# Kernel optimization log

Measured on AMD Instinct MI355X. Metric: run time of the kernel, lower is better.

Reference implementation:

```python
import jax, jax.numpy as jnp
import numpy as np
from jax import lax


def hard_sigmoid(x):
    # Keras hard_sigmoid: clip(0.2*x + 0.5, 0, 1)
    return jnp.clip(0.2 * x + 0.5, 0.0, 1.0)


def setup_inputs() -> dict:
    key = jax.random.key(0)
    ks = jax.random.split(key, 5)
    B, T, D, U, N = 256, 128, 256, 512, 2
    x = jax.random.normal(ks[0], (B, T, D), dtype=jnp.float32)
    h0 = jnp.zeros((B, U), dtype=jnp.float32)
    kernel = jax.random.normal(ks[1], (D, 5 * U), dtype=jnp.float32) * (1.0 / np.sqrt(D))
    recurrent_kernel = jax.random.normal(ks[2], (U, 4 * U), dtype=jnp.float32) * (1.0 / np.sqrt(U))
    t_kernels = jax.random.normal(ks[3], (N, U, 3 * U), dtype=jnp.float32) * (1.0 / np.sqrt(U))
    bias = jnp.zeros((2, 5 * U), dtype=jnp.float32)
    t_bias = jnp.zeros((N, 3 * U), dtype=jnp.float32)
    return {"x": x, "h0": h0, "kernel": kernel, "recurrent_kernel": recurrent_kernel,
            "t_kernels": t_kernels, "bias": bias, "t_bias": t_bias}


def reference(x, h0, kernel, recurrent_kernel, t_kernels, bias, t_bias):
    # x: [B,T,D]; h0: [B,U]; kernel: [D,5U]; recurrent_kernel: [U,4U]
    # t_kernels: [N,U,3U]; bias: [2,5U]; t_bias: [N,3U]
    U = h0.shape[-1]
    N = t_kernels.shape[0]  # static python int
    input_bias = bias[0]          # [5U]
    recurrent_bias = bias[1][:4 * U]  # [4U]

    # Precompute all input projections once: [B,T,5U]
    xg_all = jnp.einsum('btd,dg->btg', x, kernel) + input_bias

    def step(h, xg):
        # xg: [B,5U]
        xz, xr, xh, xl, xl2 = (xg[:, i * U:(i + 1) * U] for i in range(5))
        hg = h @ recurrent_kernel + recurrent_bias  # [B,4U]
        hz, hr, hhr, hl = (hg[:, i * U:(i + 1) * U] for i in range(4))
        z = hard_sigmoid(xz + hz)
        r = hard_sigmoid(xr + hr)
        hh = jnp.tanh(xh + r * hhr)  # reset_after=True convention
        h1 = z * h + (1.0 - z) * hh
        # tree-cell chain: recurrent-only GRU sub-updates
        for i in range(N):
            tg = h1 @ t_kernels[i] + t_bias[i]  # [B,3U]
            tz, tr, th = tg[:, :U], tg[:, U:2 * U], tg[:, 2 * U:3 * U]
            zt = hard_sigmoid(tz)
            rt = hard_sigmoid(tr)
            ht = jnp.tanh(rt * th)
            h1 = zt * h1 + (1.0 - zt) * ht
        # leak gates from the extra myl/myl2 kernels
        l = hard_sigmoid(xl + hl)
        h_out = l * h1 + (1.0 - l) * jnp.tanh(xl2)
        return h_out, h_out

    _, ys = lax.scan(step, h0, xg_all.transpose(1, 0, 2))  # ys: [T,B,U]
    return ys.transpose(1, 0, 2)  # [B,T,U]
```

## Files before the change

### kernel.cpp

```cpp
#include <hip/hip_runtime.h>
#include <math.h>

#define BB 256
#define TT 128
#define DD 256
#define UU 512
#define G5 (5 * UU)
#define G4 (4 * UU)
#define NBLK 256
#define GBLK 32

__device__ __forceinline__ float hsig(float x) {
    return fminf(fmaxf(0.2f * x + 0.5f, 0.0f), 1.0f);
}

__device__ __forceinline__ void st_sys(float* p, float v) {
    __hip_atomic_store(p, v, __ATOMIC_RELAXED, __HIP_MEMORY_SCOPE_SYSTEM);
}
__device__ __forceinline__ float ld_sys(const float* p) {
    return __hip_atomic_load(p, __ATOMIC_RELAXED, __HIP_MEMORY_SCOPE_SYSTEM);
}

__global__ __launch_bounds__(256) void pack_weights(
    const float* __restrict__ rk, const float* __restrict__ tk,
    float* __restrict__ rkp, float* __restrict__ tkp0, float* __restrict__ tkp1)
{
    int idx = blockIdx.x * 256 + threadIdx.x;
    int k = idx >> 11;
    int c = idx & 2047;
    int u = c >> 2;
    int g = c & 3;
    rkp[idx] = rk[k * G4 + g * UU + u];
    float t0 = 0.f, t1 = 0.f;
    if (g < 3) {
        t0 = tk[(size_t)k * (3 * UU) + g * UU + u];
        t1 = tk[(size_t)(UU + k) * (3 * UU) + g * UU + u];
    }
    tkp0[idx] = t0;
    tkp1[idx] = t1;
}

__global__ __launch_bounds__(256) void init_hT(
    const float* __restrict__ h0, float* __restrict__ hT)
{
    int idx = blockIdx.x * 256 + threadIdx.x;
    int u = idx >> 8;
    int b = idx & 255;
    hT[idx] = h0[(size_t)b * UU + u];
}

__device__ __forceinline__ void gbar(unsigned* cnt, unsigned& phase) {
    __syncthreads();
    if (threadIdx.x == 0) {
        phase += GBLK;
        __hip_atomic_fetch_add(cnt, 1u, __ATOMIC_RELAXED, __HIP_MEMORY_SCOPE_AGENT);
        while ((int)(__hip_atomic_load(cnt, __ATOMIC_RELAXED, __HIP_MEMORY_SCOPE_AGENT) - phase) < 0)
            __builtin_amdgcn_s_sleep(2);
        __builtin_amdgcn_fence(__ATOMIC_ACQUIRE, "workgroup");
    }
    __syncthreads();
    __builtin_amdgcn_sched_barrier(0);
}

__device__ __forceinline__ void rt_gemm(
    const float* __restrict__ AT,
    const float* __restrict__ Wp,
    int bm, int bn, int tid,
    float (* __restrict__ As)[36], float (* __restrict__ Ws)[80],
    float* __restrict__ RedF,
    float* __restrict__ s, int& row_out)
{
    const int lane = tid & 63;
    const int kg = tid >> 6;
    const int r8 = lane & 7;
    const int c8 = lane >> 3;
    const int akr = tid >> 3;
    const int amc = (tid & 7) * 4;
    const int wwr = tid >> 4;
    const int wwc = (tid & 15) * 4;

    const float* ap = AT + (size_t)akr * BB + bm + amc;
    const float* wp = Wp + (size_t)wwr * G4 + bn + wwc;

    float a0[4], a1[4];
#pragma unroll
    for (int j = 0; j < 4; ++j) {
        a0[j] = ld_sys(ap + j);
        a1[j] = ld_sys(ap + 32 * BB + j);
    }
    float4 w0 = *(const float4*)wp;
    float4 w1 = *(const float4*)(wp + 16 * G4);
    float4 w2 = *(const float4*)(wp + 32 * G4);
    float4 w3 = *(const float4*)(wp + 48 * G4);

    float acc[4][8];
#pragma unroll
    for (int r = 0; r < 4; ++r)
#pragma unroll
        for (int j = 0; j < 8; ++j) acc[r][j] = 0.f;

#pragma unroll 1
    for (int tile = 0; tile < 8; ++tile) {
        __syncthreads();
        As[akr][amc + 0] = a0[0]; As[akr][amc + 1] = a0[1];
        As[akr][amc + 2] = a0[2]; As[akr][amc + 3] = a0[3];
        As[akr + 32][amc + 0] = a1[0]; As[akr + 32][amc + 1] = a1[1];
        As[akr + 32][amc + 2] = a1[2]; As[akr + 32][amc + 3] = a1[3];
        *(float4*)&Ws[wwr][wwc] = w0;
        *(float4*)&Ws[wwr + 16][wwc] = w1;
        *(float4*)&Ws[wwr + 32][wwc] = w2;
        *(float4*)&Ws[wwr + 48][wwc] = w3;
        if (tile < 7) {
            ap += 64 * BB;
            wp += 64 * G4;
#pragma unroll
            for (int j = 0; j < 4; ++j) {
                a0[j] = ld_sys(ap + j);
                a1[j] = ld_sys(ap + 32 * BB + j);
            }
            w0 = *(const float4*)wp;
            w1 = *(const float4*)(wp + 16 * G4);
            w2 = *(const float4*)(wp + 32 * G4);
            w3 = *(const float4*)(wp + 48 * G4);
        }
        __syncthreads();
        const int kb = kg * 16;
#pragma unroll
        for (int q = 0; q < 16; ++q) {
            float4 av4 = *(const float4*)&As[kb + q][r8 * 4];
            float4 wv0 = *(const float4*)&Ws[kb + q][c8 * 8];
            float4 wv1 = *(const float4*)&Ws[kb + q][c8 * 8 + 4];
            float av[4] = {av4.x, av4.y, av4.z, av4.w};
            float wv[8] = {wv0.x, wv0.y, wv0.z, wv0.w, wv1.x, wv1.y, wv1.z, wv1.w};
#pragma unroll
            for (int r = 0; r < 4; ++r)
#pragma unroll
                for (int j = 0; j < 8; ++j)
                    acc[r][j] += av[r] * wv[j];
        }
    }

#pragma unroll
    for (int r = 0; r < 4; ++r)
#pragma unroll
        for (int j = 0; j < 8; ++j)
            RedF[(kg * 32 + r * 8 + j) * 64 + lane] = acc[r][j];
    __syncthreads();
#pragma unroll
    for (int j = 0; j < 8; ++j)
        s[j] = RedF[(kg * 8 + j) * 64 + lane]
             + RedF[(32 + kg * 8 + j) * 64 + lane]
             + RedF[(64 + kg * 8 + j) * 64 + lane]
             + RedF[(96 + kg * 8 + j) * 64 + lane];
    row_out = bm + r8 * 4 + kg;
}

__device__ __forceinline__ void xg_phase(
    const float* __restrict__ x, const float* __restrict__ Wxg,
    const float* __restrict__ bias0, float* __restrict__ xgdst, int t,
    int bm, int bnx, int tid,
    float (* __restrict__ As)[36], float (* __restrict__ Ws)[80],
    float* __restrict__ RedF)
{
    const int lane = tid & 63;
    const int kg = tid >> 6;
    const int r8 = lane & 7;
    const int c8 = lane >> 3;
    const int xbr = tid >> 3;
    const int xdc = (tid & 7) * 8;

    float acc[4][10];
#pragma unroll
    for (int r = 0; r < 4; ++r)
#pragma unroll
        for (int c = 0; c < 10; ++c) acc[r][c] = 0.f;

    const float* xrow = x + ((size_t)(bm + xbr) * TT + t) * DD;

#pragma unroll 1
    for (int tile = 0; tile < 4; ++tile) {
        const int k0 = tile * 64;
        float4 xa0 = *(const float4*)(xrow + k0 + xdc);
        float4 xa1 = *(const float4*)(xrow + k0 + xdc + 4);
        float4 wv[5];
#pragma unroll
        for (int l = 0; l < 5; ++l) {
            int idx = tid + l * 256;
            int wrow = idx / 20;
            int wcol = (idx % 20) * 4;
            wv[l] = *(const float4*)(Wxg + (size_t)(k0 + wrow) * G5 + bnx + wcol);
        }
        __syncthreads();
        As[xdc + 0][xbr] = xa0.x; As[xdc + 1][xbr] = xa0.y;
        As[xdc + 2][xbr] = xa0.z; As[xdc + 3][xbr] = xa0.w;
        As[xdc + 4][xbr] = xa1.x; As[xdc + 5][xbr] = xa1.y;
        As[xdc + 6][xbr] = xa1.z; As[xdc + 7][xbr] = xa1.w;
#pragma unroll
        for (int l = 0; l < 5; ++l) {
            int idx = tid + l * 256;
            int wrow = idx / 20;
            int wcol = (idx % 20) * 4;
            *(float4*)&Ws[wrow][wcol] = wv[l];
        }
        __syncthreads();
        const int kb = kg * 16;
#pragma unroll
        for (int q = 0; q < 16; ++q) {
            float4 av4 = *(const float4*)&As[kb + q][r8 * 4];
            float4 wv0 = *(const float4*)&Ws[kb + q][c8 * 8];
            float4 wv1 = *(const float4*)&Ws[kb + q][c8 * 8 + 4];
            float2 wv2 = *(const float2*)&Ws[kb + q][64 + c8 * 2];
            float av[4] = {av4.x, av4.y, av4.z, av4.w};
            float wvv[10] = {wv0.x, wv0.y, wv0.z, wv0.w,
                             wv1.x, wv1.y, wv1.z, wv1.w, wv2.x, wv2.y};
#pragma unroll
            for (int r = 0; r < 4; ++r)
#pragma unroll
                for (int c = 0; c < 10; ++c)
                    acc[r][c] += av[r] * wvv[c];
        }
    }

#pragma unroll
    for (int r = 0; r < 4; ++r)
#pragma unroll
        for (int c = 0; c < 10; ++c)
            RedF[(kg * 40 + r * 10 + c) * 64 + lane] = acc[r][c];
    __syncthreads();
    const int row = bm + r8 * 4 + kg;
#pragma unroll
    for (int c = 0; c < 10; ++c) {
        float sv = RedF[(kg * 10 + c) * 64 + lane]
                 + RedF[(40 + kg * 10 + c) * 64 + lane]
                 + RedF[(80 + kg * 10 + c) * 64 + lane]
                 + RedF[(120 + kg * 10 + c) * 64 + lane];
        int n = bnx + (c < 8 ? c8 * 8 + c : 64 + c8 * 2 + (c - 8));
        st_sys(&xgdst[(size_t)row * G5 + n], sv + bias0[n]);
    }
}

__global__ __launch_bounds__(256, 1) void scan_all(
    const float* __restrict__ x,
    const float* __restrict__ Wxg,
    const float* __restrict__ rkp,
    const float* __restrict__ tkp0,
    const float* __restrict__ tkp1,
    const float* __restrict__ bias,
    const float* __restrict__ tb,
    float* hT, float* h1aT, float* h1bT, float* prl,
    float* xg0, float* xg1, float* out, unsigned* bar)
{
    __shared__ float As[64][36];
    __shared__ float Ws[64][80];
    __shared__ float RedF[10240];

    const int tid = threadIdx.x;
    const int bid = blockIdx.x;
    const int bm = (bid >> 5) * 32;
    const int bn = (bid & 31) * 64;
    const int bnx = (bid & 31) * 80;
    const int lane = tid & 63;
    const int c8 = lane >> 3;
    const int ub = (bn >> 2) + c8 * 2;

    unsigned* cnt = bar + (bid >> 5) * 32;
    unsigned phase = 0;

    const float* bias0 = bias;
    const float* bias1 = bias + G5;
    const float* tb0 = tb;
    const float* tb1 = tb + 3 * UU;

    xg_phase(x, Wxg, bias0, xg0, 0, bm, bnx, tid, As, Ws, RedF);
    gbar(cnt, phase);

    float* xgc = xg0;
    float* xgn = xg1;

    for (int t = 0; t < TT; ++t) {
        {
            float s[8]; int row;
            rt_gemm(hT, rkp, bm, bn, tid, As, Ws, RedF, s, row);
            const float* xr_ = xgc + (size_t)row * G5;
#pragma unroll
            for (int uu = 0; uu < 2; ++uu) {
                int u = ub + uu;
                float z  = hsig(ld_sys(xr_ + u) + s[uu * 4 + 0] + bias1[u]);
                float r  = hsig(ld_sys(xr_ + UU + u) + s[uu * 4 + 1] + bias1[UU + u]);
                float hh = tanhf(ld_sys(xr_ + 2 * UU + u) + r * (s[uu * 4 + 2] + bias1[2 * UU + u]));
                float hold = ld_sys(&hT[(size_t)u * BB + row]);
                st_sys(&h1aT[(size_t)u * BB + row], z * hold + (1.f - z) * hh);
                st_sys(&prl[(size_t)row * UU + u],
                       ld_sys(xr_ + 3 * UU + u) + s[uu * 4 + 3] + bias1[3 * UU + u]);
            }
        }
        gbar(cnt, phase);

        {
            float s[8]; int row;
            rt_gemm(h1aT, tkp0, bm, bn, tid, As, Ws, RedF, s, row);
#pragma unroll
            for (int uu = 0; uu < 2; ++uu) {
                int u = ub + uu;
                float zt = hsig(s[uu * 4 + 0] + tb0[u]);
                float rt = hsig(s[uu * 4 + 1] + tb0[UU + u]);
                float ht = tanhf(rt * (s[uu * 4 + 2] + tb0[2 * UU + u]));
                float h1v = ld_sys(&h1aT[(size_t)u * BB + row]);
                st_sys(&h1bT[(size_t)u * BB + row], zt * h1v + (1.f - zt) * ht);
            }
        }
        if (t + 1 < TT)
            xg_phase(x, Wxg, bias0, xgn, t + 1, bm, bnx, tid, As, Ws, RedF);
        gbar(cnt, phase);

        {
            float s[8]; int row;
            rt_gemm(h1bT, tkp1, bm, bn, tid, As, Ws, RedF, s, row);
#pragma unroll
            for (int uu = 0; uu < 2; ++uu) {
                int u = ub + uu;
                float zt = hsig(s[uu * 4 + 0] + tb1[u]);
                float rt = hsig(s[uu * 4 + 1] + tb1[UU + u]);
                float ht = tanhf(rt * (s[uu * 4 + 2] + tb1[2 * UU + u]));
                float h1v = ld_sys(&h1bT[(size_t)u * BB + row]);
                float h2 = zt * h1v + (1.f - zt) * ht;
                float l = hsig(ld_sys(&prl[(size_t)row * UU + u]));
                float xl2 = ld_sys(&xgc[(size_t)row * G5 + 4 * UU + u]);
                float ho = l * h2 + (1.f - l) * tanhf(xl2);
                st_sys(&hT[(size_t)u * BB + row], ho);
                out[((size_t)row * TT + t) * UU + u] = ho;
            }
        }
        gbar(cnt, phase);

        float* tmp = xgc; xgc = xgn; xgn = tmp;
    }
}

extern "C" void kernel_launch(void* const* d_in, const int* in_sizes, int n_in,
                              void* d_out, int out_size, void* d_ws, size_t ws_size,
                              hipStream_t stream) {
    const float* x      = (const float*)d_in[0];
    const float* h0     = (const float*)d_in[1];
    const float* kernel = (const float*)d_in[2];
    const float* rk     = (const float*)d_in[3];
    const float* tk     = (const float*)d_in[4];
    const float* bias   = (const float*)d_in[5];
    const float* tb     = (const float*)d_in[6];
    float* out = (float*)d_out;

    unsigned* bar = (unsigned*)d_ws;
    float* base = (float*)d_ws + 256;
    float* rkp  = base;
    float* tkp0 = rkp  + (size_t)UU * G4;
    float* tkp1 = tkp0 + (size_t)UU * G4;
    float* hT   = tkp1 + (size_t)UU * G4;
    float* h1aT = hT   + (size_t)BB * UU;
    float* h1bT = h1aT + (size_t)BB * UU;
    float* prl  = h1bT + (size_t)BB * UU;
    float* xg0  = prl  + (size_t)BB * UU;
    float* xg1  = xg0  + (size_t)BB * G5;

    hipMemsetAsync(d_ws, 0, 1024, stream);
    pack_weights<<<dim3((UU * G4) / 256), dim3(256), 0, stream>>>(rk, tk, rkp, tkp0, tkp1);
    init_hT<<<dim3((BB * UU) / 256), dim3(256), 0, stream>>>(h0, hT);

    scan_all<<<dim3(NBLK), dim3(256), 0, stream>>>(
        x, kernel, rkp, tkp0, tkp1, bias, tb,
        hT, h1aT, h1bT, prl, xg0, xg1, out, bar);
}
```

Before: 9.495 ms.

## Halve batch rows per block and double the persistent grid to 512 blocks

Shrinks the per-block batch tile from 32 to 16 rows, so the persistent scan grid doubles to 512 blocks at two blocks per CU. Shared-memory tiles, register accumulators and the reduction are remapped so each thread produces one unit per row. This spreads each step's small GEMMs over more CUs and shortens per-block work between grid barriers. In exchange the recurrent weights are streamed twice as often across blocks, there are more barrier groups, and co-residency of all blocks is now required. A release fence is also added before the barrier increment.

New measurement: 14.47 ms. 52.4% more time.

```diff
diff --git a/kernel.cpp b/kernel.cpp
--- a/kernel.cpp
+++ b/kernel.cpp
@@ -7,8 +7,9 @@
 #define UU 512
 #define G5 (5 * UU)
 #define G4 (4 * UU)
-#define NBLK 256
+#define NBLK 512
 #define GBLK 32
+#define BMR 16
 
 __device__ __forceinline__ float hsig(float x) {
     return fminf(fmaxf(0.2f * x + 0.5f, 0.0f), 1.0f);
@@ -53,6 +54,7 @@
     __syncthreads();
     if (threadIdx.x == 0) {
         phase += GBLK;
+        __builtin_amdgcn_fence(__ATOMIC_RELEASE, "agent");
         __hip_atomic_fetch_add(cnt, 1u, __ATOMIC_RELAXED, __HIP_MEMORY_SCOPE_AGENT);
         while ((int)(__hip_atomic_load(cnt, __ATOMIC_RELAXED, __HIP_MEMORY_SCOPE_AGENT) - phase) < 0)
             __builtin_amdgcn_s_sleep(2);
@@ -66,46 +68,41 @@
     const float* __restrict__ AT,
     const float* __restrict__ Wp,
     int bm, int bn, int tid,
-    float (* __restrict__ As)[36], float (* __restrict__ Ws)[80],
+    float (* __restrict__ As)[20], float (* __restrict__ Ws)[80],
     float* __restrict__ RedF,
-    float* __restrict__ s, int& row_out)
+    float* __restrict__ s, int& row_out, int& u_out)
 {
     const int lane = tid & 63;
     const int kg = tid >> 6;
     const int r8 = lane & 7;
     const int c8 = lane >> 3;
-    const int akr = tid >> 3;
-    const int amc = (tid & 7) * 4;
+    const int akr = tid >> 2;
+    const int amc = (tid & 3) * 4;
     const int wwr = tid >> 4;
     const int wwc = (tid & 15) * 4;
 
     const float* ap = AT + (size_t)akr * BB + bm + amc;
     const float* wp = Wp + (size_t)wwr * G4 + bn + wwc;
 
-    float a0[4], a1[4];
-#pragma unroll
-    for (int j = 0; j < 4; ++j) {
-        a0[j] = ld_sys(ap + j);
-        a1[j] = ld_sys(ap + 32 * BB + j);
-    }
+    float a[4];
+#pragma unroll
+    for (int j = 0; j < 4; ++j) a[j] = ld_sys(ap + j);
     float4 w0 = *(const float4*)wp;
     float4 w1 = *(const float4*)(wp + 16 * G4);
     float4 w2 = *(const float4*)(wp + 32 * G4);
     float4 w3 = *(const float4*)(wp + 48 * G4);
 
-    float acc[4][8];
-#pragma unroll
-    for (int r = 0; r < 4; ++r)
+    float acc[2][8];
+#pragma unroll
+    for (int r = 0; r < 2; ++r)
 #pragma unroll
         for (int j = 0; j < 8; ++j) acc[r][j] = 0.f;
 
 #pragma unroll 1
     for (int tile = 0; tile < 8; ++tile) {
         __syncthreads();
-        As[akr][amc + 0] = a0[0]; As[akr][amc + 1] = a0[1];
-        As[akr][amc + 2] = a0[2]; As[akr][amc + 3] = a0[3];
-        As[akr + 32][amc + 0] = a1[0]; As[akr + 32][amc + 1] = a1[1];
-        As[akr + 32][amc + 2] = a1[2]; As[akr + 32][amc + 3] = a1[3];
+        float4 av4 = {a[0], a[1], a[2], a[3]};
+        *(float4*)&As[akr][amc] = av4;
         *(float4*)&Ws[wwr][wwc] = w0;
         *(float4*)&Ws[wwr + 16][wwc] = w1;
         *(float4*)&Ws[wwr + 32][wwc] = w2;
@@ -114,10 +111,7 @@
             ap += 64 * BB;
             wp += 64 * G4;
 #pragma unroll
-            for (int j = 0; j < 4; ++j) {
-                a0[j] = ld_sys(ap + j);
-                a1[j] = ld_sys(ap + 32 * BB + j);
-            }
+            for (int j = 0; j < 4; ++j) a[j] = ld_sys(ap + j);
             w0 = *(const float4*)wp;
             w1 = *(const float4*)(wp + 16 * G4);
             w2 = *(const float4*)(wp + 32 * G4);
@@ -127,51 +121,53 @@
         const int kb = kg * 16;
 #pragma unroll
         for (int q = 0; q < 16; ++q) {
-            float4 av4 = *(const float4*)&As[kb + q][r8 * 4];
+            float2 av = *(const float2*)&As[kb + q][r8 * 2];
             float4 wv0 = *(const float4*)&Ws[kb + q][c8 * 8];
             float4 wv1 = *(const float4*)&Ws[kb + q][c8 * 8 + 4];
-            float av[4] = {av4.x, av4.y, av4.z, av4.w};
             float wv[8] = {wv0.x, wv0.y, wv0.z, wv0.w, wv1.x, wv1.y, wv1.z, wv1.w};
 #pragma unroll
-            for (int r = 0; r < 4; ++r)
-#pragma unroll
-                for (int j = 0; j < 8; ++j)
-                    acc[r][j] += av[r] * wv[j];
-        }
-    }
-
-#pragma unroll
-    for (int r = 0; r < 4; ++r)
+            for (int j = 0; j < 8; ++j) {
+                acc[0][j] += av.x * wv[j];
+                acc[1][j] += av.y * wv[j];
+            }
+        }
+    }
+
+#pragma unroll
+    for (int r = 0; r < 2; ++r)
 #pragma unroll
         for (int j = 0; j < 8; ++j)
-            RedF[(kg * 32 + r * 8 + j) * 64 + lane] = acc[r][j];
+            RedF[(kg * 16 + r * 8 + j) * 64 + lane] = acc[r][j];
     __syncthreads();
-#pragma unroll
-    for (int j = 0; j < 8; ++j)
-        s[j] = RedF[(kg * 8 + j) * 64 + lane]
-             + RedF[(32 + kg * 8 + j) * 64 + lane]
-             + RedF[(64 + kg * 8 + j) * 64 + lane]
-             + RedF[(96 + kg * 8 + j) * 64 + lane];
-    row_out = bm + r8 * 4 + kg;
+    const int rr = kg & 1;
+    const int jb = (kg >> 1) * 4;
+#pragma unroll
+    for (int jj = 0; jj < 4; ++jj)
+        s[jj] = RedF[(rr * 8 + jb + jj) * 64 + lane]
+              + RedF[(16 + rr * 8 + jb + jj) * 64 + lane]
+              + RedF[(32 + rr * 8 + jb + jj) * 64 + lane]
+              + RedF[(48 + rr * 8 + jb + jj) * 64 + lane];
+    row_out = bm + r8 * 2 + rr;
+    u_out = (bn >> 2) + c8 * 2 + (kg >> 1);
 }
 
 __device__ __forceinline__ void xg_phase(
     const float* __restrict__ x, const float* __restrict__ Wxg,
     const float* __restrict__ bias0, float* __restrict__ xgdst, int t,
     int bm, int bnx, int tid,
-    float (* __restrict__ As)[36], float (* __restrict__ Ws)[80],
+    float (* __restrict__ As)[20], float (* __restrict__ Ws)[80],
     float* __restrict__ RedF)
 {
     const int lane = tid & 63;
     const int kg = tid >> 6;
     const int r8 = lane & 7;
     const int c8 = lane >> 3;
-    const int xbr = tid >> 3;
-    const int xdc = (tid & 7) * 8;
-
-    float acc[4][10];
-#pragma unroll
-    for (int r = 0; r < 4; ++r)
+    const int xbr = tid >> 4;
+    const int xdc = (tid & 15) * 4;
+
+    float acc[2][10];
+#pragma unroll
+    for (int r = 0; r < 2; ++r)
 #pragma unroll
         for (int c = 0; c < 10; ++c) acc[r][c] = 0.f;
 
@@ -180,8 +176,7 @@
 #pragma unroll 1
     for (int tile = 0; tile < 4; ++tile) {
         const int k0 = tile * 64;
-        float4 xa0 = *(const float4*)(xrow + k0 + xdc);
-        float4 xa1 = *(const float4*)(xrow + k0 + xdc + 4);
+        float4 xa = *(const float4*)(xrow + k0 + xdc);
         float4 wv[5];
 #pragma unroll
         for (int l = 0; l < 5; ++l) {
@@ -191,10 +186,8 @@
             wv[l] = *(const float4*)(Wxg + (size_t)(k0 + wrow) * G5 + bnx + wcol);
         }
         __syncthreads();
-        As[xdc + 0][xbr] = xa0.x; As[xdc + 1][xbr] = xa0.y;
-        As[xdc + 2][xbr] = xa0.z; As[xdc + 3][xbr] = xa0.w;
-        As[xdc + 4][xbr] = xa1.x; As[xdc + 5][xbr] = xa1.y;
-        As[xdc + 6][xbr] = xa1.z; As[xdc + 7][xbr] = xa1.w;
+        As[xdc + 0][xbr] = xa.x; As[xdc + 1][xbr] = xa.y;
+        As[xdc + 2][xbr] = xa.z; As[xdc + 3][xbr] = xa.w;
 #pragma unroll
         for (int l = 0; l < 5; ++l) {
             int idx = tid + l * 256;
@@ -206,40 +199,42 @@
         const int kb = kg * 16;
 #pragma unroll
         for (int q = 0; q < 16; ++q) {
-            float4 av4 = *(const float4*)&As[kb + q][r8 * 4];
+            float2 av = *(const float2*)&As[kb + q][r8 * 2];
             float4 wv0 = *(const float4*)&Ws[kb + q][c8 * 8];
             float4 wv1 = *(const float4*)&Ws[kb + q][c8 * 8 + 4];
             float2 wv2 = *(const float2*)&Ws[kb + q][64 + c8 * 2];
-            float av[4] = {av4.x, av4.y, av4.z, av4.w};
             float wvv[10] = {wv0.x, wv0.y, wv0.z, wv0.w,
                              wv1.x, wv1.y, wv1.z, wv1.w, wv2.x, wv2.y};
 #pragma unroll
-            for (int r = 0; r < 4; ++r)
-#pragma unroll
-                for (int c = 0; c < 10; ++c)
-                    acc[r][c] += av[r] * wvv[c];
-        }
-    }
-
-#pragma unroll
-    for (int r = 0; r < 4; ++r)
+            for (int c = 0; c < 10; ++c) {
+                acc[0][c] += av.x * wvv[c];
+                acc[1][c] += av.y * wvv[c];
+            }
+        }
+    }
+
+#pragma unroll
+    for (int r = 0; r < 2; ++r)
 #pragma unroll
         for (int c = 0; c < 10; ++c)
-            RedF[(kg * 40 + r * 10 + c) * 64 + lane] = acc[r][c];
+            RedF[(kg * 20 + r * 10 + c) * 64 + lane] = acc[r][c];
     __syncthreads();
-    const int row = bm + r8 * 4 + kg;
-#pragma unroll
-    for (int c = 0; c < 10; ++c) {
-        float sv = RedF[(kg * 10 + c) * 64 + lane]
-                 + RedF[(40 + kg * 10 + c) * 64 + lane]
-                 + RedF[(80 + kg * 10 + c) * 64 + lane]
-                 + RedF[(120 + kg * 10 + c) * 64 + lane];
+    const int rr = kg & 1;
+    const int cb = (kg >> 1) * 5;
+    const int row = bm + r8 * 2 + rr;
+#pragma unroll
+    for (int cc = 0; cc < 5; ++cc) {
+        int c = cb + cc;
+        float sv = RedF[(rr * 10 + c) * 64 + lane]
+                 + RedF[(20 + rr * 10 + c) * 64 + lane]
+                 + RedF[(40 + rr * 10 + c) * 64 + lane]
+                 + RedF[(60 + rr * 10 + c) * 64 + lane];
         int n = bnx + (c < 8 ? c8 * 8 + c : 64 + c8 * 2 + (c - 8));
         st_sys(&xgdst[(size_t)row * G5 + n], sv + bias0[n]);
     }
 }
 
-__global__ __launch_bounds__(256, 1) void scan_all(
+__global__ __launch_bounds__(256, 2) void scan_all(
     const float* __restrict__ x,
     const float* __restrict__ Wxg,
     const float* __restrict__ rkp,
@@ -250,18 +245,15 @@
     float* hT, float* h1aT, float* h1bT, float* prl,
     float* xg0, float* xg1, float* out, unsigned* bar)
 {
-    __shared__ float As[64][36];
+    __shared__ float As[64][20];
     __shared__ float Ws[64][80];
-    __shared__ float RedF[10240];
+    __shared__ float RedF[5120];
 
     const int tid = threadIdx.x;
     const int bid = blockIdx.x;
-    const int bm = (bid >> 5) * 32;
+    const int bm = (bid >> 5) * BMR;
     const int bn = (bid & 31) * 64;
     const int bnx = (bid & 31) * 80;
-    const int lane = tid & 63;
-    const int c8 = lane >> 3;
-    const int ub = (bn >> 2) + c8 * 2;
 
     unsigned* cnt = bar + (bid >> 5) * 32;
     unsigned phase = 0;
@@ -279,57 +271,45 @@
 
     for (int t = 0; t < TT; ++t) {
         {
-            float s[8]; int row;
-            rt_gemm(hT, rkp, bm, bn, tid, As, Ws, RedF, s, row);
+            float s[4]; int row, u;
+            rt_gemm(hT, rkp, bm, bn, tid, As, Ws, RedF, s, row, u);
             const float* xr_ = xgc + (size_t)row * G5;
-#pragma unroll
-            for (int uu = 0; uu < 2; ++uu) {
-                int u = ub + uu;
-                float z  = hsig(ld_sys(xr_ + u) + s[uu * 4 + 0] + bias1[u]);
-                float r  = hsig(ld_sys(xr_ + UU + u) + s[uu * 4 + 1] + bias1[UU + u]);
-                float hh = tanhf(ld_sys(xr_ + 2 * UU + u) + r * (s[uu * 4 + 2] + bias1[2 * UU + u]));
-                float hold = ld_sys(&hT[(size_t)u * BB + row]);
-                st_sys(&h1aT[(size_t)u * BB + row], z * hold + (1.f - z) * hh);
-                st_sys(&prl[(size_t)row * UU + u],
-                       ld_sys(xr_ + 3 * UU + u) + s[uu * 4 + 3] + bias1[3 * UU + u]);
-            }
+            float z  = hsig(ld_sys(xr_ + u) + s[0] + bias1[u]);
+            float r  = hsig(ld_sys(xr_ + UU + u) + s[1] + bias1[UU + u]);
+            float hh = tanhf(ld_sys(xr_ + 2 * UU + u) + r * (s[2] + bias1[2 * UU + u]));
+            float hold = ld_sys(&hT[(size_t)u * BB + row]);
+            st_sys(&h1aT[(size_t)u * BB + row], z * hold + (1.f - z) * hh);
+            st_sys(&prl[(size_t)row * UU + u],
+                   ld_sys(xr_ + 3 * UU + u) + s[3] + bias1[3 * UU + u]);
         }
         gbar(cnt, phase);
 
         {
-            float s[8]; int row;
-            rt_gemm(h1aT, tkp0, bm, bn, tid, As, Ws, RedF, s, row);
-#pragma unroll
-            for (int uu = 0; uu < 2; ++uu) {
-                int u = ub + uu;
-                float zt = hsig(s[uu * 4 + 0] + tb0[u]);
-                float rt = hsig(s[uu * 4 + 1] + tb0[UU + u]);
-                float ht = tanhf(rt * (s[uu * 4 + 2] + tb0[2 * UU + u]));
-                float h1v = ld_sys(&h1aT[(size_t)u * BB + row]);
-                st_sys(&h1bT[(size_t)u * BB + row], zt * h1v + (1.f - zt) * ht);
-            }
+            float s[4]; int row, u;
+            rt_gemm(h1aT, tkp0, bm, bn, tid, As, Ws, RedF, s, row, u);
+            float zt = hsig(s[0] + tb0[u]);
+            float rt = hsig(s[1] + tb0[UU + u]);
+            float ht = tanhf(rt * (s[2] + tb0[2 * UU + u]));
+            float h1v = ld_sys(&h1aT[(size_t)u * BB + row]);
+            st_sys(&h1bT[(size_t)u * BB + row], zt * h1v + (1.f - zt) * ht);
         }
         if (t + 1 < TT)
             xg_phase(x, Wxg, bias0, xgn, t + 1, bm, bnx, tid, As, Ws, RedF);
         gbar(cnt, phase);
 
         {
-            float s[8]; int row;
-            rt_gemm(h1bT, tkp1, bm, bn, tid, As, Ws, RedF, s, row);
-#pragma unroll
-            for (int uu = 0; uu < 2; ++uu) {
-                int u = ub + uu;
-                float zt = hsig(s[uu * 4 + 0] + tb1[u]);
-                float rt = hsig(s[uu * 4 + 1] + tb1[UU + u]);
-                float ht = tanhf(rt * (s[uu * 4 + 2] + tb1[2 * UU + u]));
-                float h1v = ld_sys(&h1bT[(size_t)u * BB + row]);
-                float h2 = zt * h1v + (1.f - zt) * ht;
-                float l = hsig(ld_sys(&prl[(size_t)row * UU + u]));
-                float xl2 = ld_sys(&xgc[(size_t)row * G5 + 4 * UU + u]);
-                float ho = l * h2 + (1.f - l) * tanhf(xl2);
-                st_sys(&hT[(size_t)u * BB + row], ho);
-                out[((size_t)row * TT + t) * UU + u] = ho;
-            }
+            float s[4]; int row, u;
+            rt_gemm(h1bT, tkp1, bm, bn, tid, As, Ws, RedF, s, row, u);
+            float zt = hsig(s[0] + tb1[u]);
+            float rt = hsig(s[1] + tb1[UU + u]);
+            float ht = tanhf(rt * (s[2] + tb1[2 * UU + u]));
+            float h1v = ld_sys(&h1bT[(size_t)u * BB + row]);
+            float h2 = zt * h1v + (1.f - zt) * ht;
+            float l = hsig(ld_sys(&prl[(size_t)row * UU + u]));
+            float xl2 = ld_sys(&xgc[(size_t)row * G5 + 4 * UU + u]);
+            float ho = l * h2 + (1.f - l) * tanhf(xl2);
+            st_sys(&hT[(size_t)u * BB + row], ho);
+            out[((size_t)row * TT + t) * UU + u] = ho;
         }
         gbar(cnt, phase);
 
@@ -350,7 +330,7 @@
     float* out = (float*)d_out;
 
     unsigned* bar = (unsigned*)d_ws;
-    float* base = (float*)d_ws + 256;
+    float* base = (float*)d_ws + 512;
     float* rkp  = base;
     float* tkp0 = rkp  + (size_t)UU * G4;
     float* tkp1 = tkp0 + (size_t)UU * G4;
@@ -361,7 +341,7 @@
     float* xg0  = prl  + (size_t)BB * UU;
     float* xg1  = xg0  + (size_t)BB * G5;
 
-    hipMemsetAsync(d_ws, 0, 1024, stream);
+    hipMemsetAsync(d_ws, 0, 2048, stream);
     pack_weights<<<dim3((UU * G4) / 256), dim3(256), 0, stream>>>(rk, tk, rkp, tkp0, tkp1);
     init_hT<<<dim3((BB * UU) / 256), dim3(256), 0, stream>>>(h0, hT);
 
```
